# Kernel optimization log

Hardware: AMD Instinct MI355X
Metric: run time of the kernel (lower is better)

Reference implementation:

```python
import jax, jax.numpy as jnp
import numpy as np
import math

B, T, C = 8, 2048, 1024
DIM_ATT, DIM_FFN = 1024, 4096
N_LAYER, LAYER_ID = 12, 1
EPS = 1e-5


def setup_inputs() -> dict:
    key = jax.random.key(0)
    ks = jax.random.split(key, 16)

    # deterministic init constants per RWKV source
    r01 = LAYER_ID / (N_LAYER - 1)
    r1a0 = 1.0 - LAYER_ID / N_LAYER
    ddd = (np.arange(C, dtype=np.float32) / C)[None, None, :]
    decay_speed = -5.0 + 8.0 * (np.arange(DIM_ATT, dtype=np.float32) / (DIM_ATT - 1)) ** (0.7 + 1.3 * r01)
    zigzag = (np.array([(i + 1) % 3 - 1 for i in range(DIM_ATT)], dtype=np.float32)) * 0.5

    def lin(k, out_d, in_d):
        return jax.random.normal(k, (out_d, in_d), jnp.float32) * (1.0 / math.sqrt(in_d))

    return {
        "x": jax.random.normal(ks[0], (B, T, C), jnp.float32),
        "ln1_w": jnp.ones((C,), jnp.float32),
        "ln1_b": jnp.zeros((C,), jnp.float32),
        "ln2_w": jnp.ones((C,), jnp.float32),
        "ln2_b": jnp.zeros((C,), jnp.float32),
        # time-mix (attention) params
        "att_tmk": jnp.asarray(ddd ** r1a0),
        "att_tmv": jnp.asarray(ddd ** r1a0 + 0.3 * r01),
        "att_tmr": jnp.asarray(ddd ** (0.5 * r1a0)),
        "time_decay": jnp.asarray(decay_speed),
        "time_first": jnp.asarray(np.full(DIM_ATT, math.log(0.3), np.float32) + zigzag),
        "Wk": lin(ks[1], DIM_ATT, C),
        "Wv": lin(ks[2], DIM_ATT, C),
        "Wr": lin(ks[3], DIM_ATT, C),
        "Wo": lin(ks[4], C, DIM_ATT),
        # channel-mix params
        "ffn_tmk": jnp.asarray(ddd ** r1a0),
        "ffn_tmr": jnp.asarray(ddd ** r1a0),
        "Wkey": lin(ks[5], DIM_FFN, C),
        "Wrec": lin(ks[6], C, C),
        "Wval": lin(ks[7], C, DIM_FFN),
    }


def layer_norm(x, w, b):
    mu = jnp.mean(x, axis=-1, keepdims=True)
    var = jnp.mean(jnp.square(x - mu), axis=-1, keepdims=True)
    return (x - mu) * jax.lax.rsqrt(var + EPS) * w + b


def time_shift(x):
    # xx[:, t] = x[:, t-1], zero at t=0  (nn.ZeroPad2d((0,0,1,-1)))
    return jnp.pad(x, ((0, 0), (1, 0), (0, 0)))[:, :-1, :]


def wkv(time_decay, time_first, k, v):
    # numerically stable RWKV-4 WKV recurrence, vectorized over (B, C)
    w = -jnp.exp(time_decay)  # [C]
    u = time_first            # [C]

    def step(carry, kv_t):
        aa, bb, pp = carry        # each [B, C]
        kt, vt = kv_t             # [B, C]
        ww = u + kt
        qq = jnp.maximum(pp, ww)
        e1 = jnp.exp(pp - qq)
        e2 = jnp.exp(ww - qq)
        y = (e1 * aa + e2 * vt) / (e1 * bb + e2)
        ww2 = pp + w
        qq2 = jnp.maximum(ww2, kt)
        e1b = jnp.exp(ww2 - qq2)
        e2b = jnp.exp(kt - qq2)
        return (e1b * aa + e2b * vt, e1b * bb + e2b, qq2), y

    init = (jnp.zeros_like(k[:, 0]), jnp.zeros_like(k[:, 0]),
            jnp.full_like(k[:, 0], -1e38))
    kT = jnp.swapaxes(k, 0, 1)  # [T, B, C]
    vT = jnp.swapaxes(v, 0, 1)
    _, yT = jax.lax.scan(step, init, (kT, vT))
    return jnp.swapaxes(yT, 0, 1)  # [B, T, C]


def reference(x, ln1_w, ln1_b, ln2_w, ln2_b,
              att_tmk, att_tmv, att_tmr, time_decay, time_first,
              Wk, Wv, Wr, Wo,
              ffn_tmk, ffn_tmr, Wkey, Wrec, Wval):
    # --- time-mix (attention) with residual ---
    h = layer_norm(x, ln1_w, ln1_b)
    hh = time_shift(h)
    xk = h * att_tmk + hh * (1 - att_tmk)
    xv = h * att_tmv + hh * (1 - att_tmv)
    xr = h * att_tmr + hh * (1 - att_tmr)
    k = xk @ Wk.T
    v = xv @ Wv.T
    sr = jax.nn.sigmoid(xr @ Wr.T)
    rwkv = sr * wkv(time_decay, time_first, k, v)
    x = x + rwkv @ Wo.T

    # --- channel-mix (FFN) with residual ---
    h = layer_norm(x, ln2_w, ln2_b)
    hh = time_shift(h)
    xk = h * ffn_tmk + hh * (1 - ffn_tmk)
    xr = h * ffn_tmr + hh * (1 - ffn_tmr)
    kk = jnp.square(jax.nn.relu(xk @ Wkey.T))
    kv = kk @ Wval.T
    x = x + jax.nn.sigmoid(xr @ Wrec.T) * kv
    return x
```

## Files before the change

### kernel.cpp

```cpp
#include <hip/hip_runtime.h>
#include <stdint.h>

#define B_ 8
#define T_ 2048
#define C_ 1024
#define F_ 4096
#define M_ (B_*T_)
#define NC 16
#define LCH (T_/NC)

typedef __attribute__((ext_vector_type(8))) short bf16x8;
typedef __attribute__((ext_vector_type(4))) float f32x4;

static __device__ __forceinline__ unsigned short f2bf(float f) {
    union { float f; unsigned u; } v; v.f = f;
    unsigned r = v.u + 0x7fffu + ((v.u >> 16) & 1u);
    return (unsigned short)(r >> 16);
}
static __device__ __forceinline__ float bf2f(unsigned short h) {
    union { unsigned u; float f; } v; v.u = ((unsigned)h) << 16;
    return v.f;
}

#define GLDS16(gp, lp) __builtin_amdgcn_global_load_lds( \
    (const __attribute__((address_space(1))) unsigned int*)(gp), \
    (__attribute__((address_space(3))) unsigned int*)(lp), 16, 0, 0)

#define SB0() __builtin_amdgcn_sched_barrier(0)

struct WSrc { const float* p[7]; };

__global__ __launch_bounds__(256) void k_convert(WSrc w, unsigned short* __restrict__ dst) {
    size_t e = ((size_t)blockIdx.x * 256 + threadIdx.x) * 4;
    int seg = (int)(e >> 20);
    const float* s; size_t off;
    if (seg < 5)      { s = w.p[seg]; off = e - ((size_t)seg << 20); }
    else if (seg < 9) { s = w.p[5];   off = e - (5ull << 20); }
    else              { s = w.p[6];   off = e - (9ull << 20); }
    float4 v = *(const float4*)(s + off);
    ushort4 o;
    o.x = f2bf(v.x); o.y = f2bf(v.y); o.z = f2bf(v.z); o.w = f2bf(v.w);
    *(ushort4*)(dst + e) = o;
}

template<int THREE>
__global__ __launch_bounds__(256) void k_ln_mix(
    const float* __restrict__ xin, const float* __restrict__ lw, const float* __restrict__ lb,
    const float* __restrict__ tk, const float* __restrict__ tv, const float* __restrict__ tr,
    unsigned short* __restrict__ ok, unsigned short* __restrict__ ov, unsigned short* __restrict__ orr)
{
    __shared__ float sred[4][4];
    const int m = blockIdx.x;
    const int t = m & (T_ - 1);
    const int tid = threadIdx.x;
    const int col0 = tid * 4;

    const float4 xc = *(const float4*)(xin + (size_t)m * C_ + col0);
    float4 xp = make_float4(0.f, 0.f, 0.f, 0.f);
    if (t > 0) xp = *(const float4*)(xin + (size_t)(m - 1) * C_ + col0);

    float s1 = xc.x + xc.y + xc.z + xc.w;
    float s2 = xc.x*xc.x + xc.y*xc.y + xc.z*xc.z + xc.w*xc.w;
    float s3 = xp.x + xp.y + xp.z + xp.w;
    float s4 = xp.x*xp.x + xp.y*xp.y + xp.z*xp.z + xp.w*xp.w;
    #pragma unroll
    for (int off = 32; off > 0; off >>= 1) {
        s1 += __shfl_down(s1, off);
        s2 += __shfl_down(s2, off);
        s3 += __shfl_down(s3, off);
        s4 += __shfl_down(s4, off);
    }
    const int wave = tid >> 6, lane = tid & 63;
    if (lane == 0) { sred[0][wave]=s1; sred[1][wave]=s2; sred[2][wave]=s3; sred[3][wave]=s4; }
    __syncthreads();
    const float S1 = sred[0][0]+sred[0][1]+sred[0][2]+sred[0][3];
    const float S2 = sred[1][0]+sred[1][1]+sred[1][2]+sred[1][3];
    const float S3 = sred[2][0]+sred[2][1]+sred[2][2]+sred[2][3];
    const float S4 = sred[3][0]+sred[3][1]+sred[3][2]+sred[3][3];

    const float inv = 1.0f / (float)C_;
    const float muc = S1 * inv;
    const float rc  = rsqrtf(S2 * inv - muc * muc + 1e-5f);
    const float mup = S3 * inv;
    const float rp  = rsqrtf(S4 * inv - mup * mup + 1e-5f);

    const float xcv[4] = {xc.x, xc.y, xc.z, xc.w};
    const float xpv[4] = {xp.x, xp.y, xp.z, xp.w};
    unsigned short rk[4], rv[4], rr[4];
    #pragma unroll
    for (int i = 0; i < 4; ++i) {
        const int col = col0 + i;
        const float w_ = lw[col], b_ = lb[col];
        const float h  = (xcv[i] - muc) * rc * w_ + b_;
        const float hh = (t > 0) ? (xpv[i] - mup) * rp * w_ + b_ : 0.f;
        const float ak = tk[col];
        rk[i] = f2bf(h * ak + hh * (1.f - ak));
        if (THREE) { const float av = tv[col]; rv[i] = f2bf(h * av + hh * (1.f - av)); }
        const float ar = tr[col];
        rr[i] = f2bf(h * ar + hh * (1.f - ar));
    }
    const size_t o = (size_t)m * C_ + col0;
    ushort4 u;
    u.x = rk[0]; u.y = rk[1]; u.z = rk[2]; u.w = rk[3];
    *(ushort4*)(ok + o) = u;
    if (THREE) {
        u.x = rv[0]; u.y = rv[1]; u.z = rv[2]; u.w = rv[3];
        *(ushort4*)(ov + o) = u;
    }
    u.x = rr[0]; u.y = rr[1]; u.z = rr[2]; u.w = rr[3];
    *(ushort4*)(orr + o) = u;
}

__global__ __launch_bounds__(256) void k_wkv_local(
    const unsigned short* __restrict__ kb, const unsigned short* __restrict__ vb,
    const float* __restrict__ tdec, float4* __restrict__ st)
{
    const int g = blockIdx.x * 256 + threadIdx.x;
    const int c = g & (C_ - 1);
    const int j = (g >> 10) & (NC - 1);
    const int b = g >> 14;
    const float w = -__expf(tdec[c]);
    float aa = 0.f, bb = 0.f, pp = -1e38f;
    const size_t base = ((size_t)(b * T_ + j * LCH)) * C_ + c;
    #pragma unroll 4
    for (int t = 0; t < LCH; ++t) {
        const float kt = bf2f(kb[base + (size_t)t * C_]);
        const float vt = bf2f(vb[base + (size_t)t * C_]);
        const float ww2 = pp + w;
        const float qq2 = fmaxf(ww2, kt);
        const float e1b = __expf(ww2 - qq2);
        const float e2b = __expf(kt - qq2);
        aa = e1b * aa + e2b * vt;
        bb = e1b * bb + e2b;
        pp = qq2;
    }
    st[((size_t)b * NC + j) * C_ + c] = make_float4(aa, bb, pp, 0.f);
}

__global__ __launch_bounds__(256) void k_wkv_scan(
    const unsigned short* __restrict__ kb, const unsigned short* __restrict__ vb,
    const unsigned short* __restrict__ sr,
    const float* __restrict__ tdec, const float* __restrict__ tfirst,
    const float4* __restrict__ st, unsigned short* __restrict__ p)
{
    const int g = blockIdx.x * 256 + threadIdx.x;
    const int c = g & (C_ - 1);
    const int j = (g >> 10) & (NC - 1);
    const int b = g >> 14;
    const float w = -__expf(tdec[c]);
    const float u = tfirst[c];

    float aa = 0.f, bb = 0.f, pp = -1e38f;
    for (int i = 0; i < j; ++i) {
        const float4 s = st[((size_t)b * NC + i) * C_ + c];
        const float pdec = pp + w * (float)LCH;
        const float q  = fmaxf(pdec, s.z);
        const float eA = __expf(pdec - q);
        const float eB = __expf(s.z - q);
        aa = eA * aa + eB * s.x;
        bb = eA * bb + eB * s.y;
        pp = q;
    }

    const size_t base = ((size_t)(b * T_ + j * LCH)) * C_ + c;
    #pragma unroll 4
    for (int t = 0; t < LCH; ++t) {
        const size_t idx = base + (size_t)t * C_;
        const float kt = bf2f(kb[idx]);
        const float vt = bf2f(vb[idx]);
        const float ww = u + kt;
        const float qq = fmaxf(pp, ww);
        const float e1 = __expf(pp - qq);
        const float e2 = __expf(ww - qq);
        const float y  = (e1 * aa + e2 * vt) / (e1 * bb + e2);
        p[idx] = f2bf(bf2f(sr[idx]) * y);
        const float ww2 = pp + w;
        const float qq2 = fmaxf(ww2, kt);
        const float e1b = __expf(ww2 - qq2);
        const float e2b = __expf(kt - qq2);
        aa = e1b * aa + e2b * vt;
        bb = e1b * bb + e2b;
        pp = qq2;
    }
}

static __device__ __forceinline__ void gemm_core8(
    const unsigned short* __restrict__ A, int lda,
    const unsigned short* __restrict__ Bw, int ldb,
    int K, int m0, int n0,
    unsigned short* As, unsigned short* Bs, f32x4 acc[8][4])
{
    const int tid  = threadIdx.x;
    const int w    = tid >> 6, l = tid & 63;
    const int l16  = l & 15, quad = l >> 4;
    const int wm   = w >> 2, wn = w & 3;

    const int swz_s = ((l >> 2) & 3) ^ ((l >> 4) & 3);
    const int blk_s = (l & 3) ^ swz_s;
    const unsigned short* gA0 = A  + (size_t)(m0 + w * 16 + (l >> 2)) * lda + blk_s * 8;
    const unsigned short* gA1 = gA0 + (size_t)128 * lda;
    const unsigned short* gB0 = Bw + (size_t)(n0 + w * 16 + (l >> 2)) * ldb + blk_s * 8;
    const unsigned short* gB1 = gB0 + (size_t)128 * ldb;

    auto stageA = [&](int tt, int ss) {
        const size_t ko = (size_t)tt * 32;
        GLDS16(gA0 + ko, As + ss * 8192 + w * 512);
        GLDS16(gA1 + ko, As + ss * 8192 + 4096 + w * 512);
    };
    auto stageB = [&](int tt, int ss) {
        const size_t ko = (size_t)tt * 32;
        GLDS16(gB0 + ko, Bs + ss * 8192 + w * 512);
        GLDS16(gB1 + ko, Bs + ss * 8192 + 4096 + w * 512);
    };

    const int pswz = (l16 & 3) ^ ((l16 >> 2) & 3);
    const unsigned short* aRd = As + (wm * 128 + l16) * 32 + ((quad ^ pswz) << 3);
    const unsigned short* bRd = Bs + (wn * 64  + l16) * 32 + ((quad ^ pswz) << 3);

    stageA(0, 0); stageB(0, 0);
    stageA(1, 1); stageB(1, 1);
    asm volatile("s_waitcnt vmcnt(4)" ::: "memory");
    SB0();
    __builtin_amdgcn_s_barrier();
    SB0();

    const int NT = K >> 5;
    int rs = 0, ws2 = 2;
    for (int t = 0; t < NT; ++t) {
        const unsigned short* ab = aRd + rs * 8192;
        const unsigned short* bb = bRd + rs * 8192;
        bf16x8 af[4], bf[4];

        #pragma unroll
        for (int j = 0; j < 4; ++j) bf[j] = *(const bf16x8*)(bb + j * 512);
        #pragma unroll
        for (int i = 0; i < 4; ++i) af[i] = *(const bf16x8*)(ab + i * 512);
        if (t + 2 < NT) stageA(t + 2, ws2);
        SB0();
        __builtin_amdgcn_s_barrier();
        asm volatile("s_waitcnt lgkmcnt(0)" ::: "memory");
        SB0();
        __builtin_amdgcn_s_setprio(1);
        #pragma unroll
        for (int i = 0; i < 4; ++i)
            #pragma unroll
            for (int j = 0; j < 4; ++j)
                acc[i][j] = __builtin_amdgcn_mfma_f32_16x16x32_bf16(af[i], bf[j], acc[i][j], 0, 0, 0);
        __builtin_amdgcn_s_setprio(0);
        SB0();
        __builtin_amdgcn_s_barrier();
        SB0();

        bf16x8 ag[4];
        #pragma unroll
        for (int i = 0; i < 4; ++i) ag[i] = *(const bf16x8*)(ab + (4 + i) * 512);
        if (t + 2 < NT) stageB(t + 2, ws2);
        SB0();
        __builtin_amdgcn_s_barrier();
        asm volatile("s_waitcnt lgkmcnt(0)" ::: "memory");
        SB0();
        __builtin_amdgcn_s_setprio(1);
        #pragma unroll
        for (int i = 0; i < 4; ++i)
            #pragma unroll
            for (int j = 0; j < 4; ++j)
                acc[4 + i][j] = __builtin_amdgcn_mfma_f32_16x16x32_bf16(ag[i], bf[j], acc[4 + i][j], 0, 0, 0);
        __builtin_amdgcn_s_setprio(0);
        asm volatile("s_waitcnt vmcnt(4)" ::: "memory");
        SB0();
        __builtin_amdgcn_s_barrier();
        SB0();

        rs  = (rs  == 2) ? 0 : rs + 1;
        ws2 = (ws2 == 2) ? 0 : ws2 + 1;
    }
}

template<int EPI>
__global__ __launch_bounds__(512, 2) void k_gemm(
    const unsigned short* __restrict__ A, int lda,
    const unsigned short* __restrict__ Bw, int ldb,
    int K, int N,
    float* __restrict__ outF, unsigned short* __restrict__ outH,
    const float* __restrict__ resid, const unsigned short* __restrict__ mul)
{
    __shared__ unsigned short As[3 * 8192];
    __shared__ unsigned short Bs[3 * 8192];
    f32x4 acc[8][4];
    const f32x4 zero = {0.f, 0.f, 0.f, 0.f};
    #pragma unroll
    for (int i = 0; i < 8; ++i)
        #pragma unroll
        for (int j = 0; j < 4; ++j) acc[i][j] = zero;

    const int m0 = blockIdx.x * 256, n0 = blockIdx.y * 256;
    gemm_core8(A, lda, Bw, ldb, K, m0, n0, As, Bs, acc);

    const int lane = threadIdx.x & 63, wave = threadIdx.x >> 6;
    const int quad = lane >> 4, l16 = lane & 15;
    const int wm = (wave >> 2) * 128, wn = (wave & 3) * 64;
    #pragma unroll
    for (int i = 0; i < 8; ++i) {
        const int rowb = m0 + wm + i * 16 + quad * 4;
        #pragma unroll
        for (int j = 0; j < 4; ++j) {
            const int col = n0 + wn + j * 16 + l16;
            #pragma unroll
            for (int r = 0; r < 4; ++r) {
                const size_t idx = (size_t)(rowb + r) * N + col;
                const float v = acc[i][j][r];
                if (EPI == 1)      outH[idx] = f2bf(1.f / (1.f + __expf(-v)));
                else if (EPI == 2) outF[idx] = resid[idx] + v;
                else if (EPI == 3) { const float z = v > 0.f ? v : 0.f; outH[idx] = f2bf(z * z); }
                else               outF[idx] = outF[idx] + bf2f(mul[idx]) * v;
            }
        }
    }
}

__global__ __launch_bounds__(512, 2) void k_gemm_kvr(
    const unsigned short* __restrict__ xk, const unsigned short* __restrict__ xv,
    const unsigned short* __restrict__ xr,
    const unsigned short* __restrict__ W3,
    unsigned short* __restrict__ ok, unsigned short* __restrict__ ov,
    unsigned short* __restrict__ orr)
{
    __shared__ unsigned short As[3 * 8192];
    __shared__ unsigned short Bs[3 * 8192];
    f32x4 acc[8][4];
    const f32x4 zero = {0.f, 0.f, 0.f, 0.f};
    #pragma unroll
    for (int i = 0; i < 8; ++i)
        #pragma unroll
        for (int j = 0; j < 4; ++j) acc[i][j] = zero;

    const int m0 = blockIdx.x * 256, n0 = blockIdx.y * 256;
    const int seg = n0 >> 10;
    const unsigned short* A = (seg == 0) ? xk : (seg == 1) ? xv : xr;
    unsigned short* outH    = (seg == 0) ? ok : (seg == 1) ? ov : orr;

    gemm_core8(A, C_, W3, C_, C_, m0, n0, As, Bs, acc);

    const int nl0 = n0 & (C_ - 1);
    const int lane = threadIdx.x & 63, wave = threadIdx.x >> 6;
    const int quad = lane >> 4, l16 = lane & 15;
    const int wm = (wave >> 2) * 128, wn = (wave & 3) * 64;
    #pragma unroll
    for (int i = 0; i < 8; ++i) {
        const int rowb = m0 + wm + i * 16 + quad * 4;
        #pragma unroll
        for (int j = 0; j < 4; ++j) {
            const int col = nl0 + wn + j * 16 + l16;
            #pragma unroll
            for (int r = 0; r < 4; ++r) {
                const size_t idx = (size_t)(rowb + r) * C_ + col;
                float v = acc[i][j][r];
                if (seg == 2) v = 1.f / (1.f + __expf(-v));
                outH[idx] = f2bf(v);
            }
        }
    }
}

extern "C" void kernel_launch(void* const* d_in, const int* in_sizes, int n_in,
                              void* d_out, int out_size, void* d_ws, size_t ws_size,
                              hipStream_t stream)
{
    const float* x      = (const float*)d_in[0];
    const float* ln1w   = (const float*)d_in[1];
    const float* ln1b   = (const float*)d_in[2];
    const float* ln2w   = (const float*)d_in[3];
    const float* ln2b   = (const float*)d_in[4];
    const float* atk    = (const float*)d_in[5];
    const float* atv    = (const float*)d_in[6];
    const float* atr    = (const float*)d_in[7];
    const float* tdec   = (const float*)d_in[8];
    const float* tfirst = (const float*)d_in[9];
    const float* Wk     = (const float*)d_in[10];
    const float* Wv     = (const float*)d_in[11];
    const float* Wr     = (const float*)d_in[12];
    const float* Wo     = (const float*)d_in[13];
    const float* ftk    = (const float*)d_in[14];
    const float* ftr    = (const float*)d_in[15];
    const float* Wkey   = (const float*)d_in[16];
    const float* Wrec   = (const float*)d_in[17];
    const float* Wval   = (const float*)d_in[18];
    float* out = (float*)d_out;

    char* ws = (char*)d_ws;
    const size_t MB = 1ull << 20;
    unsigned short* xk  = (unsigned short*)(ws + 0 * MB);
    unsigned short* xv  = (unsigned short*)(ws + 32 * MB);
    unsigned short* xr  = (unsigned short*)(ws + 64 * MB);
    unsigned short* sr  = (unsigned short*)(ws + 96 * MB);
    unsigned short* wb  = (unsigned short*)(ws + 128 * MB);
    float4* states      = (float4*)(ws + 0 * MB);
    unsigned short* p   = xv;
    unsigned short* xk2 = xk;
    unsigned short* xr2 = xr;
    unsigned short* s2  = sr;
    unsigned short* tmp = xv;
    unsigned short* kb  = (unsigned short*)d_out;
    unsigned short* vb  = (unsigned short*)d_out + (32*MB/2);

    unsigned short* W3_b   = wb;
    unsigned short* Wo_b   = wb + 3 * (1u << 20);
    unsigned short* Wrec_b = wb + 4 * (1u << 20);
    unsigned short* Wkey_b = wb + 5 * (1u << 20);
    unsigned short* Wval_b = wb + 9 * (1u << 20);

    WSrc wsrc; wsrc.p[0]=Wk; wsrc.p[1]=Wv; wsrc.p[2]=Wr; wsrc.p[3]=Wo;
    wsrc.p[4]=Wrec; wsrc.p[5]=Wkey; wsrc.p[6]=Wval;
    k_convert<<<dim3(13312), dim3(256), 0, stream>>>(wsrc, wb);

    k_ln_mix<1><<<dim3(M_), dim3(256), 0, stream>>>(x, ln1w, ln1b, atk, atv, atr, xk, xv, xr);

    k_gemm_kvr<<<dim3(64, 12), dim3(512), 0, stream>>>(xk, xv, xr, W3_b, kb, vb, sr);

    k_wkv_local<<<dim3(512), dim3(256), 0, stream>>>(kb, vb, tdec, states);
    k_wkv_scan<<<dim3(512), dim3(256), 0, stream>>>(kb, vb, sr, tdec, tfirst, states, p);

    k_gemm<2><<<dim3(64, 4), dim3(512), 0, stream>>>(p, 1024, Wo_b, 1024, 1024, 1024, out, (unsigned short*)nullptr, x, (const unsigned short*)nullptr);

    k_ln_mix<0><<<dim3(M_), dim3(256), 0, stream>>>(out, ln2w, ln2b, ftk, (const float*)nullptr, ftr, xk2, (unsigned short*)nullptr, xr2);

    k_gemm<1><<<dim3(64, 4), dim3(512), 0, stream>>>(xr2, 1024, Wrec_b, 1024, 1024, 1024, (float*)nullptr, s2, (const float*)nullptr, (const unsigned short*)nullptr);

    for (int f = 0; f < 4; ++f) {
        const unsigned short* WkeyF = Wkey_b + (size_t)f * 1024 * 1024;
        const unsigned short* WvalF = Wval_b + (size_t)f * 1024;
        k_gemm<3><<<dim3(64, 4), dim3(512), 0, stream>>>(xk2, 1024, WkeyF, 1024, 1024, 1024, (float*)nullptr, tmp, (const float*)nullptr, (const unsigned short*)nullptr);
        k_gemm<4><<<dim3(64, 4), dim3(512), 0, stream>>>(tmp, 1024, WvalF, 4096, 1024, 1024, out, (unsigned short*)nullptr, (const float*)nullptr, s2);
    }
}
```

Baseline: 970.2 us.

## Restructure GEMM core to BK=64 double-buffered pipeline with four-phase schedule

Replaces the triple-buffered BK=32 GEMM mainloop with a double-buffered BK=64 loop that splits each K-tile into four MFMA phases. Global-to-LDS prefetches of the next tile are interleaved across the phases, and a new 8-way XOR swizzle is meant to avoid LDS bank conflicts. LDS use grows to 128KB per block, so launch bounds drop to one block per CU. The aim is fewer barriers per unit of K and more MFMA work per synchronisation, at the cost of occupancy.

```diff
diff --git a/kernel.cpp b/kernel.cpp
--- a/kernel.cpp
+++ b/kernel.cpp
@@ -27,6 +27,7 @@
     (__attribute__((address_space(3))) unsigned int*)(lp), 16, 0, 0)
 
 #define SB0() __builtin_amdgcn_sched_barrier(0)
+#define MFMA_BF16(a, b, c) __builtin_amdgcn_mfma_f32_16x16x32_bf16((a), (b), (c), 0, 0, 0)
 
 struct WSrc { const float* p[7]; };
 
@@ -184,108 +185,174 @@
     }
 }
 
-static __device__ __forceinline__ void gemm_core8(
+static __device__ __forceinline__ void gemm_core256(
     const unsigned short* __restrict__ A, int lda,
     const unsigned short* __restrict__ Bw, int ldb,
     int K, int m0, int n0,
     unsigned short* As, unsigned short* Bs, f32x4 acc[8][4])
 {
     const int tid  = threadIdx.x;
-    const int w    = tid >> 6, l = tid & 63;
+    const int l    = tid & 63;
     const int l16  = l & 15, quad = l >> 4;
+    const int w    = tid >> 6;
     const int wm   = w >> 2, wn = w & 3;
 
-    const int swz_s = ((l >> 2) & 3) ^ ((l >> 4) & 3);
-    const int blk_s = (l & 3) ^ swz_s;
-    const unsigned short* gA0 = A  + (size_t)(m0 + w * 16 + (l >> 2)) * lda + blk_s * 8;
-    const unsigned short* gA1 = gA0 + (size_t)128 * lda;
-    const unsigned short* gB0 = Bw + (size_t)(n0 + w * 16 + (l >> 2)) * ldb + blk_s * 8;
-    const unsigned short* gB1 = gB0 + (size_t)128 * ldb;
-
-    auto stageA = [&](int tt, int ss) {
-        const size_t ko = (size_t)tt * 32;
-        GLDS16(gA0 + ko, As + ss * 8192 + w * 512);
-        GLDS16(gA1 + ko, As + ss * 8192 + 4096 + w * 512);
+    const int sr_ = tid >> 3;
+    const int sb_ = (tid & 7) ^ (sr_ & 7);
+    const unsigned short* gA = A  + (size_t)(m0 + sr_) * lda + sb_ * 8;
+    const unsigned short* gB = Bw + (size_t)(n0 + sr_) * ldb + sb_ * 8;
+
+    auto stA = [&](int tt, int ss, int u) {
+        GLDS16(gA + (size_t)u * 64 * lda + tt * 64, As + ss * 16384 + u * 4096 + w * 512);
     };
-    auto stageB = [&](int tt, int ss) {
-        const size_t ko = (size_t)tt * 32;
-        GLDS16(gB0 + ko, Bs + ss * 8192 + w * 512);
-        GLDS16(gB1 + ko, Bs + ss * 8192 + 4096 + w * 512);
+    auto stB = [&](int tt, int ss, int u) {
+        GLDS16(gB + (size_t)u * 64 * ldb + tt * 64, Bs + ss * 16384 + u * 4096 + w * 512);
     };
 
-    const int pswz = (l16 & 3) ^ ((l16 >> 2) & 3);
-    const unsigned short* aRd = As + (wm * 128 + l16) * 32 + ((quad ^ pswz) << 3);
-    const unsigned short* bRd = Bs + (wn * 64  + l16) * 32 + ((quad ^ pswz) << 3);
-
-    stageA(0, 0); stageB(0, 0);
-    stageA(1, 1); stageB(1, 1);
-    asm volatile("s_waitcnt vmcnt(4)" ::: "memory");
+    const int swz = l16 & 7;
+    const unsigned short* aR = As + (wm * 128 + l16) * 64;
+    const unsigned short* bR = Bs + (wn * 64  + l16) * 64;
+    const int o0 = ((0 + quad) ^ swz) * 8;
+    const int o1 = ((4 + quad) ^ swz) * 8;
+
+    stA(0, 0, 0); stA(0, 0, 2);
+    stB(0, 0, 0); stB(0, 0, 1); stB(0, 0, 2); stB(0, 0, 3);
+    stA(0, 0, 1); stA(0, 0, 3);
+    asm volatile("s_waitcnt vmcnt(0)" ::: "memory");
     SB0();
     __builtin_amdgcn_s_barrier();
     SB0();
 
-    const int NT = K >> 5;
-    int rs = 0, ws2 = 2;
+    const int NT = K >> 6;
     for (int t = 0; t < NT; ++t) {
-        const unsigned short* ab = aRd + rs * 8192;
-        const unsigned short* bb = bRd + rs * 8192;
-        bf16x8 af[4], bf[4];
-
-        #pragma unroll
-        for (int j = 0; j < 4; ++j) bf[j] = *(const bf16x8*)(bb + j * 512);
-        #pragma unroll
-        for (int i = 0; i < 4; ++i) af[i] = *(const bf16x8*)(ab + i * 512);
-        if (t + 2 < NT) stageA(t + 2, ws2);
-        SB0();
-        __builtin_amdgcn_s_barrier();
-        asm volatile("s_waitcnt lgkmcnt(0)" ::: "memory");
-        SB0();
-        __builtin_amdgcn_s_setprio(1);
-        #pragma unroll
-        for (int i = 0; i < 4; ++i)
-            #pragma unroll
-            for (int j = 0; j < 4; ++j)
-                acc[i][j] = __builtin_amdgcn_mfma_f32_16x16x32_bf16(af[i], bf[j], acc[i][j], 0, 0, 0);
-        __builtin_amdgcn_s_setprio(0);
-        SB0();
-        __builtin_amdgcn_s_barrier();
-        SB0();
-
-        bf16x8 ag[4];
-        #pragma unroll
-        for (int i = 0; i < 4; ++i) ag[i] = *(const bf16x8*)(ab + (4 + i) * 512);
-        if (t + 2 < NT) stageB(t + 2, ws2);
-        SB0();
-        __builtin_amdgcn_s_barrier();
-        asm volatile("s_waitcnt lgkmcnt(0)" ::: "memory");
-        SB0();
-        __builtin_amdgcn_s_setprio(1);
-        #pragma unroll
-        for (int i = 0; i < 4; ++i)
-            #pragma unroll
-            for (int j = 0; j < 4; ++j)
-                acc[4 + i][j] = __builtin_amdgcn_mfma_f32_16x16x32_bf16(ag[i], bf[j], acc[4 + i][j], 0, 0, 0);
-        __builtin_amdgcn_s_setprio(0);
-        asm volatile("s_waitcnt vmcnt(4)" ::: "memory");
-        SB0();
-        __builtin_amdgcn_s_barrier();
-        SB0();
-
-        rs  = (rs  == 2) ? 0 : rs + 1;
-        ws2 = (ws2 == 2) ? 0 : ws2 + 1;
+        const int rs = t & 1, ns = rs ^ 1;
+        const unsigned short* ab = aR + rs * 16384;
+        const unsigned short* bb = bR + rs * 16384;
+        const bool pf = (t + 1 < NT);
+        bf16x8 b0[4], b1[4];
+
+        {
+            bf16x8 a0[2], a1[2];
+            #pragma unroll
+            for (int j = 0; j < 4; ++j) {
+                b0[j] = *(const bf16x8*)(bb + j * 1024 + o0);
+                b1[j] = *(const bf16x8*)(bb + j * 1024 + o1);
+            }
+            #pragma unroll
+            for (int i = 0; i < 2; ++i) {
+                a0[i] = *(const bf16x8*)(ab + i * 1024 + o0);
+                a1[i] = *(const bf16x8*)(ab + i * 1024 + o1);
+            }
+            if (pf) { stA(t + 1, ns, 0); stA(t + 1, ns, 2); }
+            SB0();
+            __builtin_amdgcn_s_barrier();
+            asm volatile("s_waitcnt lgkmcnt(0)" ::: "memory");
+            SB0();
+            __builtin_amdgcn_s_setprio(1);
+            #pragma unroll
+            for (int i = 0; i < 2; ++i)
+                #pragma unroll
+                for (int j = 0; j < 4; ++j) {
+                    acc[i][j] = MFMA_BF16(a0[i], b0[j], acc[i][j]);
+                    acc[i][j] = MFMA_BF16(a1[i], b1[j], acc[i][j]);
+                }
+            __builtin_amdgcn_s_setprio(0);
+            SB0();
+            __builtin_amdgcn_s_barrier();
+            SB0();
+        }
+
+        {
+            bf16x8 a0[2], a1[2];
+            #pragma unroll
+            for (int i = 0; i < 2; ++i) {
+                a0[i] = *(const bf16x8*)(ab + (2 + i) * 1024 + o0);
+                a1[i] = *(const bf16x8*)(ab + (2 + i) * 1024 + o1);
+            }
+            if (pf) { stB(t + 1, ns, 0); stB(t + 1, ns, 1); stB(t + 1, ns, 2); stB(t + 1, ns, 3); }
+            SB0();
+            __builtin_amdgcn_s_barrier();
+            asm volatile("s_waitcnt lgkmcnt(0)" ::: "memory");
+            SB0();
+            __builtin_amdgcn_s_setprio(1);
+            #pragma unroll
+            for (int i = 0; i < 2; ++i)
+                #pragma unroll
+                for (int j = 0; j < 4; ++j) {
+                    acc[2 + i][j] = MFMA_BF16(a0[i], b0[j], acc[2 + i][j]);
+                    acc[2 + i][j] = MFMA_BF16(a1[i], b1[j], acc[2 + i][j]);
+                }
+            __builtin_amdgcn_s_setprio(0);
+            asm volatile("s_waitcnt vmcnt(6)" ::: "memory");
+            SB0();
+            __builtin_amdgcn_s_barrier();
+            SB0();
+        }
+
+        {
+            bf16x8 a0[2], a1[2];
+            #pragma unroll
+            for (int i = 0; i < 2; ++i) {
+                a0[i] = *(const bf16x8*)(ab + (4 + i) * 1024 + o0);
+                a1[i] = *(const bf16x8*)(ab + (4 + i) * 1024 + o1);
+            }
+            if (pf) { stA(t + 1, ns, 1); stA(t + 1, ns, 3); }
+            SB0();
+            __builtin_amdgcn_s_barrier();
+            asm volatile("s_waitcnt lgkmcnt(0)" ::: "memory");
+            SB0();
+            __builtin_amdgcn_s_setprio(1);
+            #pragma unroll
+            for (int i = 0; i < 2; ++i)
+                #pragma unroll
+                for (int j = 0; j < 4; ++j) {
+                    acc[4 + i][j] = MFMA_BF16(a0[i], b0[j], acc[4 + i][j]);
+                    acc[4 + i][j] = MFMA_BF16(a1[i], b1[j], acc[4 + i][j]);
+                }
+            __builtin_amdgcn_s_setprio(0);
+            SB0();
+            __builtin_amdgcn_s_barrier();
+            SB0();
+        }
+
+        {
+            bf16x8 a0[2], a1[2];
+            #pragma unroll
+            for (int i = 0; i < 2; ++i) {
+                a0[i] = *(const bf16x8*)(ab + (6 + i) * 1024 + o0);
+                a1[i] = *(const bf16x8*)(ab + (6 + i) * 1024 + o1);
+            }
+            SB0();
+            __builtin_amdgcn_s_barrier();
+            asm volatile("s_waitcnt lgkmcnt(0)" ::: "memory");
+            SB0();
+            __builtin_amdgcn_s_setprio(1);
+            #pragma unroll
+            for (int i = 0; i < 2; ++i)
+                #pragma unroll
+                for (int j = 0; j < 4; ++j) {
+                    acc[6 + i][j] = MFMA_BF16(a0[i], b0[j], acc[6 + i][j]);
+                    acc[6 + i][j] = MFMA_BF16(a1[i], b1[j], acc[6 + i][j]);
+                }
+            __builtin_amdgcn_s_setprio(0);
+            asm volatile("s_waitcnt vmcnt(2)" ::: "memory");
+            SB0();
+            __builtin_amdgcn_s_barrier();
+            SB0();
+        }
     }
 }
 
 template<int EPI>
-__global__ __launch_bounds__(512, 2) void k_gemm(
+__global__ __launch_bounds__(512, 1) void k_gemm(
     const unsigned short* __restrict__ A, int lda,
     const unsigned short* __restrict__ Bw, int ldb,
     int K, int N,
     float* __restrict__ outF, unsigned short* __restrict__ outH,
     const float* __restrict__ resid, const unsigned short* __restrict__ mul)
 {
-    __shared__ unsigned short As[3 * 8192];
-    __shared__ unsigned short Bs[3 * 8192];
+    __shared__ unsigned short As[2 * 16384];
+    __shared__ unsigned short Bs[2 * 16384];
     f32x4 acc[8][4];
     const f32x4 zero = {0.f, 0.f, 0.f, 0.f};
     #pragma unroll
@@ -294,7 +361,7 @@
         for (int j = 0; j < 4; ++j) acc[i][j] = zero;
 
     const int m0 = blockIdx.x * 256, n0 = blockIdx.y * 256;
-    gemm_core8(A, lda, Bw, ldb, K, m0, n0, As, Bs, acc);
+    gemm_core256(A, lda, Bw, ldb, K, m0, n0, As, Bs, acc);
 
     const int lane = threadIdx.x & 63, wave = threadIdx.x >> 6;
     const int quad = lane >> 4, l16 = lane & 15;
@@ -318,15 +385,15 @@
     }
 }
 
-__global__ __launch_bounds__(512, 2) void k_gemm_kvr(
+__global__ __launch_bounds__(512, 1) void k_gemm_kvr(
     const unsigned short* __restrict__ xk, const unsigned short* __restrict__ xv,
     const unsigned short* __restrict__ xr,
     const unsigned short* __restrict__ W3,
     unsigned short* __restrict__ ok, unsigned short* __restrict__ ov,
     unsigned short* __restrict__ orr)
 {
-    __shared__ unsigned short As[3 * 8192];
-    __shared__ unsigned short Bs[3 * 8192];
+    __shared__ unsigned short As[2 * 16384];
+    __shared__ unsigned short Bs[2 * 16384];
     f32x4 acc[8][4];
     const f32x4 zero = {0.f, 0.f, 0.f, 0.f};
     #pragma unroll
@@ -339,7 +406,7 @@
     const unsigned short* A = (seg == 0) ? xk : (seg == 1) ? xv : xr;
     unsigned short* outH    = (seg == 0) ? ok : (seg == 1) ? ov : orr;
 
-    gemm_core8(A, C_, W3, C_, C_, m0, n0, As, Bs, acc);
+    gemm_core256(A, C_, W3, C_, C_, m0, n0, As, Bs, acc);
 
     const int nl0 = n0 & (C_ - 1);
     const int lane = threadIdx.x & 63, wave = threadIdx.x >> 6;
```

Result: faster. 943.3 us (-2.8%).
